# Kernel tuning notes

Hardware: AMD Instinct MI355X
Metric: run time of the kernel (lower is better)

Reference implementation:

```python
import jax, jax.numpy as jnp
import numpy as np

C = 256
CR = 32  # C // nc_reduce

def setup_inputs() -> dict:
    key = jax.random.key(0)
    ks = jax.random.split(key, 8)
    B, H, W = 4, 64, 64
    x = jax.random.normal(ks[0], (B, C, H, W), dtype=jnp.float32)
    s_in = 1.0 / np.sqrt(C)
    Wq = jax.random.uniform(ks[1], (CR, C), jnp.float32, -s_in, s_in)
    bq = jax.random.uniform(ks[2], (CR,), jnp.float32, -s_in, s_in)
    Wk = jax.random.uniform(ks[3], (CR, C), jnp.float32, -s_in, s_in)
    bk = jax.random.uniform(ks[4], (CR,), jnp.float32, -s_in, s_in)
    Wv = jax.random.uniform(ks[5], (C, C), jnp.float32, -s_in, s_in)
    bv = jax.random.uniform(ks[6], (C,), jnp.float32, -s_in, s_in)
    gamma = jnp.zeros((1,), dtype=jnp.float32)
    return {"x": x, "Wq": Wq, "bq": bq, "Wk": Wk, "bk": bk,
            "Wv": Wv, "bv": bv, "gamma": gamma}

def reference(x, Wq, bq, Wk, bk, Wv, bv, gamma):
    B, Cc, H, W = x.shape
    N = H * W
    xf = x.reshape(B, Cc, N)                       # [B, C, N]
    # 1x1 convs == per-position channel projections
    q = jnp.einsum('dc,bcn->bdn', Wq, xf) + bq[None, :, None]  # [B, CR, N]
    k = jnp.einsum('dc,bcn->bdn', Wk, xf) + bk[None, :, None]  # [B, CR, N]
    v = jnp.einsum('dc,bcn->bdn', Wv, xf) + bv[None, :, None]  # [B, C, N]
    # energy[b,i,j] = q[:, :, i] . k[:, :, j]  (no scaling, as in source)
    energy = jnp.einsum('bdi,bdj->bij', q, k)      # [B, N, N]
    attn = jax.nn.softmax(energy, axis=-1)
    # out[b,c,i] = sum_j v[b,c,j] * attn[b,i,j]
    outv = jnp.einsum('bcj,bij->bci', v, attn)     # [B, C, N]
    out = gamma[0] * outv.reshape(B, Cc, H, W) + x
    return out
```

## Files before the change

### kernel.cpp

```cpp
#include <hip/hip_runtime.h>
#include <hip/hip_bf16.h>

#define NB 4
#define CCH 256
#define CRD 32
#define NN 4096

typedef __attribute__((ext_vector_type(8))) short short8;
typedef __attribute__((ext_vector_type(4))) float floatx4;
typedef __attribute__((ext_vector_type(4))) int intx4;
typedef __attribute__((ext_vector_type(2))) unsigned int uintx2;

__device__ __forceinline__ unsigned short f2bf(float f) {
  unsigned u = __builtin_bit_cast(unsigned, f);
  u += 0x7FFFu + ((u >> 16) & 1u);
  return (unsigned short)(u >> 16);
}

__device__ __forceinline__ unsigned short f2bf_c(float f) {
  f = fminf(fmaxf(f, -1.0e4f), 1.0e4f);
  unsigned u = __builtin_bit_cast(unsigned, f);
  u += 0x7FFFu + ((u >> 16) & 1u);
  return (unsigned short)(u >> 16);
}

__device__ __forceinline__ unsigned pack2c(float a, float b) {
  return (unsigned)f2bf_c(a) | ((unsigned)f2bf_c(b) << 16);
}

__device__ __forceinline__ float sat(float v) {
  return fminf(fmaxf(v, -1.0e30f), 1.0e30f);
}

__device__ __forceinline__ short8 ld_frag_g(const unsigned short* p) {
  return __builtin_bit_cast(short8, *(const intx4*)p);
}

__global__ __launch_bounds__(256) void gemm_qkv_fused(
    const float* __restrict__ x,
    const float* __restrict__ Wq, const float* __restrict__ bq,
    const float* __restrict__ Wk, const float* __restrict__ bk,
    const float* __restrict__ Wv, const float* __restrict__ bv,
    unsigned short* __restrict__ qT, unsigned short* __restrict__ kT,
    unsigned short* __restrict__ vv)
{
  __shared__ __align__(16) unsigned short xs[64 * 264];
  __shared__ __align__(16) unsigned short ws[64 * 264];

  const int tid  = threadIdx.x;
  const int wave = tid >> 6;
  const int lane = tid & 63;
  const int lq   = lane >> 4;
  const int lm   = lane & 15;
  const int n0   = blockIdx.x << 6;
  const int mg   = blockIdx.y;
  const int b    = blockIdx.z;

  {
    const int nn = lane;
    const int cg = wave;
    const float* xb = x + ((size_t)b << 20) + n0 + nn;
#pragma unroll
    for (int it = 0; it < 16; ++it) {
      const int c0 = it * 16 + cg * 4;
      const float v0 = xb[(size_t)(c0 + 0) << 12];
      const float v1 = xb[(size_t)(c0 + 1) << 12];
      const float v2 = xb[(size_t)(c0 + 2) << 12];
      const float v3 = xb[(size_t)(c0 + 3) << 12];
      uintx2 u;
      u[0] = pack2c(v0, v1);
      u[1] = pack2c(v2, v3);
      *(uintx2*)(xs + nn * 264 + c0) = u;
    }
  }

  const int mt_lo = mg ? 3 : 0;
  const int mt_hi = mg ? 5 : 3;

  for (int mt = mt_lo; mt < mt_hi; ++mt) {
#pragma unroll
    for (int i = 0; i < 16; ++i) {
      const int u  = i * 256 + tid;
      const int m  = u >> 6;
      const int o4 = (u & 63) * 4;
      const float* src = (mt == 0)
          ? (m < 32 ? Wq + (size_t)m * CCH : Wk + (size_t)(m - 32) * CCH)
          : Wv + (size_t)((mt - 1) * 64 + m) * CCH;
      const floatx4 f = *(const floatx4*)(src + o4);
      uintx2 uu;
      uu[0] = pack2c(f[0], f[1]);
      uu[1] = pack2c(f[2], f[3]);
      *(uintx2*)(ws + m * 264 + o4) = uu;
    }
    __syncthreads();

    floatx4 acc[4];
#pragma unroll
    for (int t = 0; t < 4; ++t) acc[t] = (floatx4){0.f, 0.f, 0.f, 0.f};

#pragma unroll
    for (int k0 = 0; k0 < 8; ++k0) {
      short8 af[4];
#pragma unroll
      for (int ms = 0; ms < 4; ++ms)
        af[ms] = __builtin_bit_cast(short8,
            *(const intx4*)(ws + (ms * 16 + lm) * 264 + k0 * 32 + lq * 8));
      const short8 bf = __builtin_bit_cast(short8,
          *(const intx4*)(xs + (wave * 16 + lm) * 264 + k0 * 32 + lq * 8));
#pragma unroll
      for (int ms = 0; ms < 4; ++ms)
        acc[ms] = __builtin_amdgcn_mfma_f32_16x16x32_bf16(af[ms], bf,
                                                          acc[ms], 0, 0, 0);
    }
    __syncthreads();

    if (mt == 0) {
      const int n = n0 + wave * 16 + lm;
#pragma unroll
      for (int ms = 0; ms < 4; ++ms) {
        const int d0 = (ms & 1) * 16 + lq * 4;
        const float* bias = (ms < 2) ? bq : bk;
        unsigned short* dst = (ms < 2) ? qT : kT;
        uintx2 u;
        u[0] = pack2c(acc[ms][0] + bias[d0],     acc[ms][1] + bias[d0 + 1]);
        u[1] = pack2c(acc[ms][2] + bias[d0 + 2], acc[ms][3] + bias[d0 + 3]);
        *(uintx2*)(dst + (size_t)(b * NN + n) * CRD + d0) = u;
      }
    } else {
      const int cb = (mt - 1) * 64;
      unsigned short* vb2 = ws;
#pragma unroll
      for (int ms = 0; ms < 4; ++ms)
#pragma unroll
        for (int r = 0; r < 4; ++r) {
          const int c = ms * 16 + lq * 4 + r;
          vb2[c * 64 + wave * 16 + lm] = f2bf_c(acc[ms][r] + bv[cb + c]);
        }
      __syncthreads();
#pragma unroll
      for (int it = 0; it < 2; ++it) {
        const int u = it * 256 + tid;
        const int m = u >> 3;
        const int o = (u & 7) * 8;
        *(intx4*)(vv + (size_t)(b * CCH + cb + m) * NN + n0 + o) =
            *(const intx4*)(vb2 + m * 64 + o);
      }
      __syncthreads();
    }
  }
}

__global__ __launch_bounds__(256) void attn_kernel(
    const float* __restrict__ x, const float* __restrict__ gamma_p,
    const unsigned short* __restrict__ qT, const unsigned short* __restrict__ kT,
    const unsigned short* __restrict__ vv, float* __restrict__ out)
{
  __shared__ __align__(16) unsigned char smem[65536 + 2 * 4352];

  const int tid  = threadIdx.x;
  const int cs   = tid >> 6;
  const int lane = tid & 63;
  const int lq   = lane >> 4;
  const int lm   = lane & 15;
  const int xcd = blockIdx.x & 7;
  const int p   = blockIdx.x >> 3;
  const int b   = xcd >> 1;
  const int i0  = (((xcd & 1) << 6) | p) << 5;

  const unsigned short* kTb = kT + (size_t)b * NN * CRD;
  const unsigned short* vb  = vv + (size_t)b * CCH * NN;

  short8 qf[2];
#pragma unroll
  for (int f = 0; f < 2; ++f)
    qf[f] = ld_frag_g(qT + (size_t)(b * NN + i0 + f * 16 + lm) * CRD + lq * 8);

  int vs_g[8];
  int vs_off[8];
#pragma unroll
  for (int m = 0; m < 8; ++m) {
    const int u  = m * 256 + tid;
    const int c  = u >> 3;
    const int jb = u & 7;
    vs_g[m]   = c * NN + jb * 8;
    vs_off[m] = c * 128 + ((jb ^ (c & 7)) * 16);
  }

  floatx4 acc[8];
#pragma unroll
  for (int t = 0; t < 8; ++t) acc[t] = (floatx4){0.f, 0.f, 0.f, 0.f};
  float lsum[8] = {0.f, 0.f, 0.f, 0.f, 0.f, 0.f, 0.f, 0.f};

  intx4 vreg[8];
#pragma unroll
  for (int m = 0; m < 8; ++m)
    vreg[m] = *(const intx4*)(vb + vs_g[m]);
  short8 kf = ld_frag_g(kTb + (size_t)(cs * 16 + lm) * CRD + lq * 8);

  const floatx4 zf = {0.f, 0.f, 0.f, 0.f};

#pragma unroll 1
  for (int k = 0; k < 64; ++k) {
    unsigned char* vbuf = smem + ((k & 1) << 15);
    unsigned char* pb   = smem + 65536 + (k & 1) * 4352;

#pragma unroll
    for (int m = 0; m < 8; ++m)
      *(intx4*)(vbuf + vs_off[m]) = vreg[m];

#pragma unroll
    for (int f = 0; f < 2; ++f) {
      floatx4 S = __builtin_amdgcn_mfma_f32_16x16x32_bf16(qf[f], kf, zf, 0, 0, 0);
#pragma unroll
      for (int r = 0; r < 4; ++r) {
        const float pv = __expf(fminf(fmaxf(S[r], -40.f), 40.f));
        lsum[f * 4 + r] += pv;
        *(unsigned short*)(pb + (f * 16 + lq * 4 + r) * 136 +
                           ((cs * 16 + lm) << 1)) = f2bf(pv);
      }
    }

    __syncthreads();

    if (k < 63) {
      const int j0n = (k + 1) << 6;
#pragma unroll
      for (int m = 0; m < 8; ++m)
        vreg[m] = *(const intx4*)(vb + vs_g[m] + j0n);
      kf = ld_frag_g(kTb + (size_t)(j0n + cs * 16 + lm) * CRD + lq * 8);
    }

    __builtin_amdgcn_s_setprio(1);
#pragma unroll
    for (int ks = 0; ks < 2; ++ks) {
      short8 pf[2];
#pragma unroll
      for (int f = 0; f < 2; ++f) {
        const unsigned char* pa = pb + (f * 16 + lm) * 136 + ks * 64 + lq * 16;
        struct U128 { unsigned long long a, b; } pp;
        pp.a = *(const unsigned long long*)pa;
        pp.b = *(const unsigned long long*)(pa + 8);
        pf[f] = __builtin_bit_cast(short8, pp);
      }
#pragma unroll
      for (int nt = 0; nt < 4; ++nt) {
        const int c = cs * 64 + nt * 16 + lm;
        const short8 vf = __builtin_bit_cast(
            short8,
            *(const intx4*)(vbuf + c * 128 + (((ks * 4 + lq) ^ (lm & 7)) * 16)));
#pragma unroll
        for (int f = 0; f < 2; ++f)
          acc[f * 4 + nt] = __builtin_amdgcn_mfma_f32_16x16x32_bf16(
              pf[f], vf, acc[f * 4 + nt], 0, 0, 0);
      }
    }
    __builtin_amdgcn_s_setprio(0);
  }

#pragma unroll
  for (int e = 0; e < 8; ++e) {
    float v = lsum[e];
    v += __shfl_xor(v, 1);
    v += __shfl_xor(v, 2);
    v += __shfl_xor(v, 4);
    v += __shfl_xor(v, 8);
    lsum[e] = v;
  }
  __syncthreads();
  float* lbuf = (float*)smem;
  {
    const int base = (cs * 64 + lane) * 8;
#pragma unroll
    for (int e = 0; e < 8; ++e) lbuf[base + e] = lsum[e];
  }
  __syncthreads();
  float inv[8];
#pragma unroll
  for (int e = 0; e < 8; ++e) {
    float v = 0.f;
#pragma unroll
    for (int q = 0; q < 4; ++q)
      v += lbuf[(q * 64 + lane) * 8 + e];
    inv[e] = 1.0f / v;
  }

  const float gm = gamma_p[0];
#pragma unroll
  for (int f = 0; f < 2; ++f)
#pragma unroll
    for (int nt = 0; nt < 4; ++nt) {
      const int c = cs * 64 + nt * 16 + lm;
      const int i = i0 + f * 16 + lq * 4;
      const size_t idx = (size_t)(b * CCH + c) * NN + i;
      const floatx4 xv = *(const floatx4*)(x + idx);
      floatx4 o;
#pragma unroll
      for (int r = 0; r < 4; ++r)
        o[r] = gm * sat(acc[f * 4 + nt][r] * inv[f * 4 + r]) + xv[r];
      *(floatx4*)(out + idx) = o;
    }
}

extern "C" void kernel_launch(void* const* d_in, const int* in_sizes, int n_in,
                              void* d_out, int out_size, void* d_ws, size_t ws_size,
                              hipStream_t stream) {
  (void)in_sizes; (void)n_in; (void)out_size; (void)ws_size;
  const float* x     = (const float*)d_in[0];
  const float* Wq    = (const float*)d_in[1];
  const float* bq    = (const float*)d_in[2];
  const float* Wk    = (const float*)d_in[3];
  const float* bk    = (const float*)d_in[4];
  const float* Wv    = (const float*)d_in[5];
  const float* bv    = (const float*)d_in[6];
  const float* gamma = (const float*)d_in[7];

  unsigned short* qT = (unsigned short*)d_ws;
  unsigned short* kT = qT + (size_t)NB * NN * CRD;
  unsigned short* vv = kT + (size_t)NB * NN * CRD;

  gemm_qkv_fused<<<dim3(64, 2, 4), 256, 0, stream>>>(x, Wq, bq, Wk, bk, Wv, bv,
                                                     qT, kT, vv);
  attn_kernel<<<dim3(512, 1, 1), 256, 0, stream>>>(x, gamma, qT, kT, vv,
                                                   (float*)d_out);
}
```

Measured before the change: 169.7 us.

## Restructure attention kernel to split keys across waves with register-direct V fragments

The attention kernel now uses 512-thread blocks covering 64 query rows. Each wave owns a slice of keys and half the channels, and V fragments are loaded straight from global memory into registers, replacing the LDS staging and per-iteration block barriers. Probabilities are packed into MFMA operands in registers through a transposed S computation, so the P LDS round trip disappears. Partial outputs from the four key-split waves are reduced through LDS in serialized rounds before the fused epilogue. This trades higher register pressure (32 accumulators per lane) and a final reduction for fewer syncs and less LDS traffic.

New measurement: 241.5 us. +42.3%, slower.

```diff
diff --git a/kernel.cpp b/kernel.cpp
--- a/kernel.cpp
+++ b/kernel.cpp
@@ -150,155 +150,176 @@
   }
 }
 
-__global__ __launch_bounds__(256) void attn_kernel(
+__global__ __launch_bounds__(512, 2) void attn_kernel(
     const float* __restrict__ x, const float* __restrict__ gamma_p,
     const unsigned short* __restrict__ qT, const unsigned short* __restrict__ kT,
     const unsigned short* __restrict__ vv, float* __restrict__ out)
 {
-  __shared__ __align__(16) unsigned char smem[65536 + 2 * 4352];
+  __shared__ __align__(16) float olds[64 * 264];
+  __shared__ float lsumlds[4][64];
+  __shared__ float invlds[64];
 
   const int tid  = threadIdx.x;
-  const int cs   = tid >> 6;
+  const int wave = tid >> 6;
+  const int jw   = wave & 3;
+  const int ch   = wave >> 2;
   const int lane = tid & 63;
   const int lq   = lane >> 4;
   const int lm   = lane & 15;
-  const int xcd = blockIdx.x & 7;
-  const int p   = blockIdx.x >> 3;
-  const int b   = xcd >> 1;
-  const int i0  = (((xcd & 1) << 6) | p) << 5;
+  const int xcd  = blockIdx.x & 7;
+  const int pos  = blockIdx.x >> 3;
+  const int b    = xcd >> 1;
+  const int i0   = (((xcd & 1) << 5) | pos) << 6;
 
   const unsigned short* kTb = kT + (size_t)b * NN * CRD;
   const unsigned short* vb  = vv + (size_t)b * CCH * NN;
 
-  short8 qf[2];
-#pragma unroll
-  for (int f = 0; f < 2; ++f)
+  short8 qf[4];
+#pragma unroll
+  for (int f = 0; f < 4; ++f)
     qf[f] = ld_frag_g(qT + (size_t)(b * NN + i0 + f * 16 + lm) * CRD + lq * 8);
 
-  int vs_g[8];
-  int vs_off[8];
-#pragma unroll
-  for (int m = 0; m < 8; ++m) {
-    const int u  = m * 256 + tid;
-    const int c  = u >> 3;
-    const int jb = u & 7;
-    vs_g[m]   = c * NN + jb * 8;
-    vs_off[m] = c * 128 + ((jb ^ (c & 7)) * 16);
-  }
-
-  floatx4 acc[8];
-#pragma unroll
-  for (int t = 0; t < 8; ++t) acc[t] = (floatx4){0.f, 0.f, 0.f, 0.f};
-  float lsum[8] = {0.f, 0.f, 0.f, 0.f, 0.f, 0.f, 0.f, 0.f};
-
-  intx4 vreg[8];
-#pragma unroll
-  for (int m = 0; m < 8; ++m)
-    vreg[m] = *(const intx4*)(vb + vs_g[m]);
-  short8 kf = ld_frag_g(kTb + (size_t)(cs * 16 + lm) * CRD + lq * 8);
+  const unsigned short* vrow[8];
+#pragma unroll
+  for (int cf = 0; cf < 8; ++cf)
+    vrow[cf] = vb + (size_t)(ch * 128 + cf * 16 + lm) * NN + lq * 4;
+
+  floatx4 acc[8][4];
+#pragma unroll
+  for (int cf = 0; cf < 8; ++cf)
+#pragma unroll
+    for (int f = 0; f < 4; ++f) acc[cf][f] = (floatx4){0.f, 0.f, 0.f, 0.f};
+  float lsum[4] = {0.f, 0.f, 0.f, 0.f};
 
   const floatx4 zf = {0.f, 0.f, 0.f, 0.f};
 
+  short8 kfp[2][2];
+#pragma unroll
+  for (int jt = 0; jt < 2; ++jt)
+    kfp[0][jt] = ld_frag_g(kTb + (size_t)(jw * 32 + jt * 16 + lm) * CRD + lq * 8);
+
+#pragma unroll 2
+  for (int t = 0; t < 32; ++t) {
+    const int jwb = t * 128 + jw * 32;
+
+    uintx2 vr[8][2];
+#pragma unroll
+    for (int cf = 0; cf < 4; ++cf) {
+      vr[cf][0] = *(const uintx2*)(vrow[cf] + jwb);
+      vr[cf][1] = *(const uintx2*)(vrow[cf] + jwb + 16);
+    }
+
+    if (t < 31) {
+      const int jnb = jwb + 128;
+#pragma unroll
+      for (int jt = 0; jt < 2; ++jt)
+        kfp[(t + 1) & 1][jt] =
+            ld_frag_g(kTb + (size_t)(jnb + jt * 16 + lm) * CRD + lq * 8);
+    }
+
+    short8 pf[4];
+#pragma unroll
+    for (int f = 0; f < 4; ++f) {
+      unsigned pw[4];
+#pragma unroll
+      for (int jt = 0; jt < 2; ++jt) {
+        const floatx4 S = __builtin_amdgcn_mfma_f32_16x16x32_bf16(
+            kfp[t & 1][jt], qf[f], zf, 0, 0, 0);
+        float p0 = __expf(fminf(fmaxf(S[0], -40.f), 40.f));
+        float p1 = __expf(fminf(fmaxf(S[1], -40.f), 40.f));
+        float p2 = __expf(fminf(fmaxf(S[2], -40.f), 40.f));
+        float p3 = __expf(fminf(fmaxf(S[3], -40.f), 40.f));
+        lsum[f] += (p0 + p1) + (p2 + p3);
+        pw[jt * 2 + 0] = (unsigned)f2bf(p0) | ((unsigned)f2bf(p1) << 16);
+        pw[jt * 2 + 1] = (unsigned)f2bf(p2) | ((unsigned)f2bf(p3) << 16);
+      }
+      intx4 pi;
+      pi[0] = (int)pw[0]; pi[1] = (int)pw[1];
+      pi[2] = (int)pw[2]; pi[3] = (int)pw[3];
+      pf[f] = __builtin_bit_cast(short8, pi);
+    }
+
+#pragma unroll
+    for (int cf = 4; cf < 8; ++cf) {
+      vr[cf][0] = *(const uintx2*)(vrow[cf] + jwb);
+      vr[cf][1] = *(const uintx2*)(vrow[cf] + jwb + 16);
+    }
+
+    __builtin_amdgcn_s_setprio(1);
+#pragma unroll
+    for (int cf = 0; cf < 8; ++cf) {
+      intx4 vi;
+      vi[0] = (int)vr[cf][0][0]; vi[1] = (int)vr[cf][0][1];
+      vi[2] = (int)vr[cf][1][0]; vi[3] = (int)vr[cf][1][1];
+      const short8 vf = __builtin_bit_cast(short8, vi);
+#pragma unroll
+      for (int f = 0; f < 4; ++f)
+        acc[cf][f] = __builtin_amdgcn_mfma_f32_16x16x32_bf16(
+            vf, pf[f], acc[cf][f], 0, 0, 0);
+    }
+    __builtin_amdgcn_s_setprio(0);
+  }
+
+#pragma unroll
+  for (int f = 0; f < 4; ++f) {
+    float v = lsum[f];
+    v += __shfl_xor(v, 16);
+    v += __shfl_xor(v, 32);
+    lsum[f] = v;
+  }
+  if (ch == 0 && lq == 0) {
+#pragma unroll
+    for (int f = 0; f < 4; ++f) lsumlds[jw][f * 16 + lm] = lsum[f];
+  }
+  __syncthreads();
+
 #pragma unroll 1
-  for (int k = 0; k < 64; ++k) {
-    unsigned char* vbuf = smem + ((k & 1) << 15);
-    unsigned char* pb   = smem + 65536 + (k & 1) * 4352;
-
-#pragma unroll
-    for (int m = 0; m < 8; ++m)
-      *(intx4*)(vbuf + vs_off[m]) = vreg[m];
-
-#pragma unroll
-    for (int f = 0; f < 2; ++f) {
-      floatx4 S = __builtin_amdgcn_mfma_f32_16x16x32_bf16(qf[f], kf, zf, 0, 0, 0);
-#pragma unroll
-      for (int r = 0; r < 4; ++r) {
-        const float pv = __expf(fminf(fmaxf(S[r], -40.f), 40.f));
-        lsum[f * 4 + r] += pv;
-        *(unsigned short*)(pb + (f * 16 + lq * 4 + r) * 136 +
-                           ((cs * 16 + lm) << 1)) = f2bf(pv);
-      }
-    }
-
+  for (int rnd = 0; rnd < 4; ++rnd) {
+    if (jw == rnd) {
+#pragma unroll
+      for (int cf = 0; cf < 8; ++cf)
+#pragma unroll
+        for (int f = 0; f < 4; ++f) {
+          const int i  = f * 16 + lm;
+          const int cw = (ch * 128 + cf * 16 + lq * 4) ^ (lm << 2);
+          float* dst = &olds[i * 264 + cw];
+          if (rnd == 0) {
+            *(floatx4*)dst = acc[cf][f];
+          } else {
+            floatx4 ov = *(const floatx4*)dst;
+            ov = ov + acc[cf][f];
+            *(floatx4*)dst = ov;
+          }
+        }
+    }
     __syncthreads();
-
-    if (k < 63) {
-      const int j0n = (k + 1) << 6;
-#pragma unroll
-      for (int m = 0; m < 8; ++m)
-        vreg[m] = *(const intx4*)(vb + vs_g[m] + j0n);
-      kf = ld_frag_g(kTb + (size_t)(j0n + cs * 16 + lm) * CRD + lq * 8);
-    }
-
-    __builtin_amdgcn_s_setprio(1);
-#pragma unroll
-    for (int ks = 0; ks < 2; ++ks) {
-      short8 pf[2];
-#pragma unroll
-      for (int f = 0; f < 2; ++f) {
-        const unsigned char* pa = pb + (f * 16 + lm) * 136 + ks * 64 + lq * 16;
-        struct U128 { unsigned long long a, b; } pp;
-        pp.a = *(const unsigned long long*)pa;
-        pp.b = *(const unsigned long long*)(pa + 8);
-        pf[f] = __builtin_bit_cast(short8, pp);
-      }
-#pragma unroll
-      for (int nt = 0; nt < 4; ++nt) {
-        const int c = cs * 64 + nt * 16 + lm;
-        const short8 vf = __builtin_bit_cast(
-            short8,
-            *(const intx4*)(vbuf + c * 128 + (((ks * 4 + lq) ^ (lm & 7)) * 16)));
-#pragma unroll
-        for (int f = 0; f < 2; ++f)
-          acc[f * 4 + nt] = __builtin_amdgcn_mfma_f32_16x16x32_bf16(
-              pf[f], vf, acc[f * 4 + nt], 0, 0, 0);
-      }
-    }
-    __builtin_amdgcn_s_setprio(0);
-  }
-
-#pragma unroll
-  for (int e = 0; e < 8; ++e) {
-    float v = lsum[e];
-    v += __shfl_xor(v, 1);
-    v += __shfl_xor(v, 2);
-    v += __shfl_xor(v, 4);
-    v += __shfl_xor(v, 8);
-    lsum[e] = v;
-  }
+  }
+
+  if (tid < 64)
+    invlds[tid] = 1.0f / (lsumlds[0][tid] + lsumlds[1][tid] +
+                          lsumlds[2][tid] + lsumlds[3][tid]);
   __syncthreads();
-  float* lbuf = (float*)smem;
-  {
-    const int base = (cs * 64 + lane) * 8;
-#pragma unroll
-    for (int e = 0; e < 8; ++e) lbuf[base + e] = lsum[e];
-  }
-  __syncthreads();
-  float inv[8];
-#pragma unroll
-  for (int e = 0; e < 8; ++e) {
-    float v = 0.f;
-#pragma unroll
-    for (int q = 0; q < 4; ++q)
-      v += lbuf[(q * 64 + lane) * 8 + e];
-    inv[e] = 1.0f / v;
-  }
 
   const float gm = gamma_p[0];
 #pragma unroll
-  for (int f = 0; f < 2; ++f)
-#pragma unroll
-    for (int nt = 0; nt < 4; ++nt) {
-      const int c = cs * 64 + nt * 16 + lm;
-      const int i = i0 + f * 16 + lq * 4;
-      const size_t idx = (size_t)(b * CCH + c) * NN + i;
-      const floatx4 xv = *(const floatx4*)(x + idx);
-      floatx4 o;
-#pragma unroll
-      for (int r = 0; r < 4; ++r)
-        o[r] = gm * sat(acc[f * 4 + nt][r] * inv[f * 4 + r]) + xv[r];
-      *(floatx4*)(out + idx) = o;
-    }
+  for (int pass = 0; pass < 8; ++pass) {
+    const int c  = pass * 32 + (tid >> 4);
+    const int i4 = (tid & 15) * 4;
+    floatx4 ov;
+#pragma unroll
+    for (int e = 0; e < 4; ++e) {
+      const int i = i4 + e;
+      ov[e] = olds[i * 264 + (c ^ ((i & 15) << 2))];
+    }
+    const floatx4 iv = *(const floatx4*)&invlds[i4];
+    const size_t idx = (size_t)(b * CCH + c) * NN + i0 + i4;
+    const floatx4 xv = *(const floatx4*)(x + idx);
+    floatx4 o;
+#pragma unroll
+    for (int e = 0; e < 4; ++e)
+      o[e] = gm * sat(ov[e] * iv[e]) + xv[e];
+    *(floatx4*)(out + idx) = o;
+  }
 }
 
 extern "C" void kernel_launch(void* const* d_in, const int* in_sizes, int n_in,
@@ -320,6 +341,6 @@
 
   gemm_qkv_fused<<<dim3(64, 2, 4), 256, 0, stream>>>(x, Wq, bq, Wk, bk, Wv, bv,
                                                      qT, kT, vv);
-  attn_kernel<<<dim3(512, 1, 1), 256, 0, stream>>>(x, gamma, qT, kT, vv,
+  attn_kernel<<<dim3(256, 1, 1), 512, 0, stream>>>(x, gamma, qT, kT, vv,
                                                    (float*)d_out);
 }
```
